# Performance work log

Hardware: AMD Instinct MI355X
Metric: run time of the kernel (lower is better)

Reference implementation:

```python
import jax, jax.numpy as jnp
import numpy as np

ALPHA = 0.2  # LeakyReLU negative slope
NEG = -9e15


def _gat_heads(x, adj_mask, W, a):
    # x: (B,N,F); W: (H,F,O); a: (H,2O); adj_mask: (B,N,N) bool
    O = W.shape[-1]
    Wh = jnp.einsum('bnf,hfo->bhno', x, W)            # (B,H,N,O)
    e1 = jnp.einsum('bhno,ho->bhn', Wh, a[:, :O])     # Wh @ a[:O]
    e2 = jnp.einsum('bhno,ho->bhn', Wh, a[:, O:])     # Wh @ a[O:]
    e = jax.nn.leaky_relu(e1[:, :, :, None] + e2[:, :, None, :], ALPHA)  # (B,H,N,N)
    e = jnp.where(adj_mask[:, None], e, NEG)
    attn = jax.nn.softmax(e, axis=-1)
    return jnp.einsum('bhnm,bhmo->bhno', attn, Wh)    # (B,H,N,O)


def _gat_block(x, adj_mask, non_pad_mask, W_heads, a_heads, W_out, a_out):
    # multi-head layer, concat=True -> elu per head, then concat on feature dim
    h = jax.nn.elu(_gat_heads(x, adj_mask, W_heads, a_heads))  # (B,H,N,O)
    B, H, N, O = h.shape
    h = jnp.transpose(h, (0, 2, 1, 3)).reshape(B, N, H * O)
    h = h * non_pad_mask
    # out layer: single head, concat=False (no inner elu)
    h = _gat_heads(h, adj_mask, W_out[None], a_out[None])[:, 0]  # (B,N,noutput)
    h = h * non_pad_mask
    return jax.nn.elu(h)


def setup_inputs() -> dict:
    key = jax.random.key(0)
    ks = jax.random.split(key, 8)
    B, N = 32, 256
    vocab, F, O, H, OUT = 200, 300, 256, 8, 512
    fea = jax.random.randint(ks[0], (B, N), 0, vocab, dtype=jnp.int32)
    adj = jax.random.randint(ks[1], (B, N, N), 0, 2, dtype=jnp.int32)
    non_pad_mask = jnp.ones((B, N, 1), dtype=jnp.float32)
    embed = jax.random.normal(ks[2], (vocab, F), dtype=jnp.float32)
    W_heads = jax.random.normal(ks[3], (H, F, O), dtype=jnp.float32) / np.sqrt(F)
    a_heads = jax.random.normal(ks[4], (H, 2 * O), dtype=jnp.float32) / np.sqrt(2 * O)
    W_out = jax.random.normal(ks[5], (H * O, OUT), dtype=jnp.float32) / np.sqrt(H * O)
    a_out = jax.random.normal(ks[6], (2 * OUT,), dtype=jnp.float32) / np.sqrt(2 * OUT)
    return {"fea": fea, "adj": adj, "non_pad_mask": non_pad_mask, "embed": embed,
            "W_heads": W_heads, "a_heads": a_heads, "W_out": W_out, "a_out": a_out}


def reference(fea, adj, non_pad_mask, embed, W_heads, a_heads, W_out, a_out):
    adj_mask = adj > 0
    x = embed[fea]  # (B,N,F)
    # GAT_num = 1; dropout is identity in eval mode
    x = _gat_block(x, adj_mask, non_pad_mask, W_heads, a_heads, W_out, a_out)
    return x  # (B, N, 512)
```

## Files before the change

kernel.cpp:

```cpp
#include <hip/hip_runtime.h>
#include <math.h>


typedef _Float16 f16;
typedef __attribute__((ext_vector_type(8))) _Float16 f16x8;
typedef __attribute__((ext_vector_type(4))) _Float16 f16x4;
typedef __attribute__((ext_vector_type(4))) float f32x4;

__device__ __forceinline__ void async16(const void* g, void* lds) {
  __builtin_amdgcn_global_load_lds(
      (const __attribute__((address_space(1))) void*)g,
      (__attribute__((address_space(3))) void*)lds, 16, 0, 0);
}

__global__ void k_prep_x(const int* __restrict__ fea, const float* __restrict__ embed,
                         f16* __restrict__ x16) {
  int row = blockIdx.x;
  int t = threadIdx.x;
  int tok = fea[row];
  float v = (t < 300) ? embed[tok * 300 + t] : 0.f;
  x16[(size_t)row * 320 + t] = (f16)v;
}

__global__ void k_prep_wc(const float* __restrict__ W, f16* __restrict__ WcT) {
  __shared__ float tile[32][33];
  int bx = blockIdx.x, by = blockIdx.y, h = blockIdx.z;
  int tid = threadIdx.x;
  int c = tid & 31, q = tid >> 5;
#pragma unroll
  for (int i = 0; i < 4; ++i) {
    int tt = q + i * 8;
    int t = bx * 32 + tt;
    float v = (t < 300) ? W[((size_t)h * 300 + t) * 256 + by * 32 + c] : 0.f;
    tile[tt][c] = v;
  }
  __syncthreads();
#pragma unroll
  for (int i = 0; i < 4; ++i) {
    int oo = q + i * 8;
    int gc = h * 256 + by * 32 + oo;
    WcT[(size_t)gc * 320 + bx * 32 + c] = (f16)tile[c][oo];
  }
}

__global__ void k_prep_wo(const float* __restrict__ W, f16* __restrict__ WoT) {
  __shared__ float tile[32][33];
  int bx = blockIdx.x, by = blockIdx.y;
  int tid = threadIdx.x;
  int c = tid & 31, q = tid >> 5;
#pragma unroll
  for (int i = 0; i < 4; ++i) {
    int kk = q + i * 8;
    tile[kk][c] = W[((size_t)bx * 32 + kk) * 512 + by * 32 + c];
  }
  __syncthreads();
#pragma unroll
  for (int i = 0; i < 4; ++i) {
    int oo = q + i * 8;
    WoT[((size_t)by * 32 + oo) * 2048 + bx * 32 + c] = (f16)tile[c][oo];
  }
}

template <int KDIM, int NCOLS>
__global__ __launch_bounds__(256, 4) void k_gemm1(const f16* __restrict__ A,
                                                  const f16* __restrict__ BT,
                                                  f16* __restrict__ outT,
                                                  const float* __restrict__ avec,
                                                  float* __restrict__ e1,
                                                  float* __restrict__ e2) {
  __shared__ f16 As[128 * 32];
  __shared__ f16 Bs[128 * 32];
  const int by = blockIdx.x, bx = blockIdx.y;
  const int tid = threadIdx.x;
  const int wave = tid >> 6, lane = tid & 63;
  const int wm = wave >> 1, wn = wave & 1;
  const int lrow = lane & 15, quad = lane >> 4;
  const int srow = lane >> 2;
  const int scol = ((lane & 3) ^ ((lane >> 3) & 3)) * 8;
  const int sq = (quad ^ ((lrow >> 1) & 3)) * 8;

  f32x4 acc[4][4] = {};
  const f16* Ag = A + (size_t)by * 128 * KDIM;
  const f16* Bg = BT + (size_t)bx * 128 * KDIM;

  for (int k0 = 0; k0 < KDIM; k0 += 32) {
    __syncthreads();
#pragma unroll
    for (int j = 0; j < 2; ++j) {
      const int r0 = wave * 32 + j * 16;
      async16(Ag + (size_t)(r0 + srow) * KDIM + k0 + scol, &As[r0 * 32]);
      async16(Bg + (size_t)(r0 + srow) * KDIM + k0 + scol, &Bs[r0 * 32]);
    }
    __syncthreads();
    f16x8 af[4], bf[4];
#pragma unroll
    for (int t = 0; t < 4; ++t) {
      af[t] = *(const f16x8*)&As[(wm * 64 + t * 16 + lrow) * 32 + sq];
      bf[t] = *(const f16x8*)&Bs[(wn * 64 + t * 16 + lrow) * 32 + sq];
    }
#pragma unroll
    for (int mt = 0; mt < 4; ++mt)
#pragma unroll
      for (int nt = 0; nt < 4; ++nt)
        acc[mt][nt] = __builtin_amdgcn_mfma_f32_16x16x32_f16(af[mt], bf[nt], acc[mt][nt], 0, 0, 0);
  }

  const int b = (by * 128) >> 8;
  const int nbase0 = (by * 128) & 255;
#pragma unroll
  for (int mt = 0; mt < 4; ++mt) {
    const int nb = nbase0 + wm * 64 + mt * 16 + quad * 4;
#pragma unroll
    for (int nt = 0; nt < 4; ++nt) {
      const int gc = bx * 128 + wn * 64 + nt * 16 + lrow;
      f16x4 v;
#pragma unroll
      for (int r = 0; r < 4; ++r) v[r] = (f16)acc[mt][nt][r];
      *(f16x4*)&outT[((size_t)b * NCOLS + gc) * 256 + nb] = v;
    }
  }

  float a1v[4], a2v[4];
#pragma unroll
  for (int nt = 0; nt < 4; ++nt) {
    const int gc = bx * 128 + wn * 64 + nt * 16 + lrow;
    int hh = gc >> 8, oo = gc & 255;
    a1v[nt] = avec[hh * 512 + oo];
    a2v[nt] = avec[hh * 512 + 256 + oo];
  }
  const int hblk = (bx * 128) >> 8;
  const int ebase = (b * 8 + hblk) * 256;
#pragma unroll
  for (int mt = 0; mt < 4; ++mt) {
    float s1[4] = {0.f, 0.f, 0.f, 0.f}, s2[4] = {0.f, 0.f, 0.f, 0.f};
#pragma unroll
    for (int nt = 0; nt < 4; ++nt)
#pragma unroll
      for (int r = 0; r < 4; ++r) {
        s1[r] += acc[mt][nt][r] * a1v[nt];
        s2[r] += acc[mt][nt][r] * a2v[nt];
      }
#pragma unroll
    for (int r = 0; r < 4; ++r)
#pragma unroll
      for (int m = 1; m < 16; m <<= 1) {
        s1[r] += __shfl_xor(s1[r], m);
        s2[r] += __shfl_xor(s2[r], m);
      }
    if (lrow == 0) {
      const int nb = nbase0 + wm * 64 + mt * 16 + quad * 4;
#pragma unroll
      for (int r = 0; r < 4; ++r) {
        atomicAdd(&e1[ebase + nb + r], s1[r]);
        atomicAdd(&e2[ebase + nb + r], s2[r]);
      }
    }
  }
}

__global__ __launch_bounds__(256, 4) void k_gemm_sk(const f16* __restrict__ A,
                                                    const f16* __restrict__ BT,
                                                    f16* __restrict__ outSK) {
  __shared__ f16 As[128 * 32];
  __shared__ f16 Bs[64 * 32];
  const int by = blockIdx.x, bx = blockIdx.y, kz = blockIdx.z;
  const int tid = threadIdx.x;
  const int wave = tid >> 6, lane = tid & 63;
  const int wm = wave >> 1, wn = wave & 1;
  const int lrow = lane & 15, quad = lane >> 4;
  const int srow = lane >> 2;
  const int scol = ((lane & 3) ^ ((lane >> 3) & 3)) * 8;
  const int sq = (quad ^ ((lrow >> 1) & 3)) * 8;

  f32x4 acc[4][2] = {};
  const f16* Ag = A + (size_t)by * 128 * 2048;
  const f16* Bg = BT + (size_t)bx * 64 * 2048;
  const int kbeg = kz * 1024;

  for (int k0 = kbeg; k0 < kbeg + 1024; k0 += 32) {
    __syncthreads();
#pragma unroll
    for (int j = 0; j < 2; ++j) {
      const int r0 = wave * 32 + j * 16;
      async16(Ag + (size_t)(r0 + srow) * 2048 + k0 + scol, &As[r0 * 32]);
    }
    {
      const int r0 = wave * 16;
      async16(Bg + (size_t)(r0 + srow) * 2048 + k0 + scol, &Bs[r0 * 32]);
    }
    __syncthreads();
    f16x8 af[4], bf[2];
#pragma unroll
    for (int t = 0; t < 4; ++t)
      af[t] = *(const f16x8*)&As[(wm * 64 + t * 16 + lrow) * 32 + sq];
#pragma unroll
    for (int t = 0; t < 2; ++t)
      bf[t] = *(const f16x8*)&Bs[(wn * 32 + t * 16 + lrow) * 32 + sq];
#pragma unroll
    for (int mt = 0; mt < 4; ++mt)
#pragma unroll
      for (int nt = 0; nt < 2; ++nt)
        acc[mt][nt] = __builtin_amdgcn_mfma_f32_16x16x32_f16(af[mt], bf[nt], acc[mt][nt], 0, 0, 0);
  }

  const int b = (by * 128) >> 8;
  const int nbase0 = (by * 128) & 255;
  f16* dst = outSK + (size_t)kz * 32 * 512 * 256;
#pragma unroll
  for (int mt = 0; mt < 4; ++mt) {
    const int nb = nbase0 + wm * 64 + mt * 16 + quad * 4;
#pragma unroll
    for (int nt = 0; nt < 2; ++nt) {
      const int gc = bx * 64 + wn * 32 + nt * 16 + lrow;
      f16x4 v;
#pragma unroll
      for (int r = 0; r < 4; ++r) v[r] = (f16)acc[mt][nt][r];
      *(f16x4*)&dst[((size_t)b * 512 + gc) * 256 + nb] = v;
    }
  }
}

__global__ void k_comb(const f16* __restrict__ sk, const float* __restrict__ ao,
                       f16* __restrict__ Wh2T, float* __restrict__ e12,
                       float* __restrict__ e22) {
  int oc = blockIdx.x;
  int b = blockIdx.y;
  int n = threadIdx.x;
  const f16* b0 = sk + ((size_t)b * 512 + oc * 64) * 256 + n;
  const f16* b1 = b0 + (size_t)32 * 512 * 256;
  f16* wbase = Wh2T + ((size_t)b * 512 + oc * 64) * 256 + n;
  float s1 = 0.f, s2 = 0.f;
#pragma unroll 8
  for (int j = 0; j < 64; ++j) {
    float v = (float)b0[(size_t)j * 256] + (float)b1[(size_t)j * 256];
    int o2 = oc * 64 + j;
    s1 += v * ao[o2];
    s2 += v * ao[512 + o2];
    wbase[(size_t)j * 256] = (f16)v;
  }
  atomicAdd(&e12[b * 256 + n], s1);
  atomicAdd(&e22[b * 256 + n], s2);
}

#define PSTRIDE 264

__global__ __launch_bounds__(256, 4) void k_attn1(
    const f16* __restrict__ WhT, const float* __restrict__ e1g, const float* __restrict__ e2g,
    const int* __restrict__ adj, const float* __restrict__ npm, f16* __restrict__ h1) {
  int h = blockIdx.x, b = blockIdx.y, nt0 = blockIdx.z;
  int bh = b * 8 + h;
  int n0 = nt0 * 64;
  __shared__ f16 P[64 * PSTRIDE];
  int tid = threadIdx.x;
  int wave = tid >> 6, lane = tid & 63;

  float4 e2v = *(const float4*)&e2g[bh * 256 + lane * 4];
  float e2m = fmaxf(fmaxf(e2v.x, e2v.y), fmaxf(e2v.z, e2v.w));
#pragma unroll
  for (int m = 1; m < 64; m <<= 1) e2m = fmaxf(e2m, __shfl_xor(e2m, m));
#pragma unroll 4
  for (int i = 0; i < 16; ++i) {
    int row = i * 4 + wave;
    int gn = b * 256 + n0 + row;
    float er = e1g[bh * 256 + n0 + row];
    float sh = er + e2m;
    sh = sh > 0.f ? sh : 0.2f * sh;
    int4 aj = *(const int4*)&adj[(size_t)gn * 256 + lane * 4];
    float p0, p1, p2, p3;
    {
      float v = er + e2v.x; v = v > 0.f ? v : 0.2f * v;
      p0 = aj.x ? __expf(v - sh) : 0.f;
      v = er + e2v.y; v = v > 0.f ? v : 0.2f * v;
      p1 = aj.y ? __expf(v - sh) : 0.f;
      v = er + e2v.z; v = v > 0.f ? v : 0.2f * v;
      p2 = aj.z ? __expf(v - sh) : 0.f;
      v = er + e2v.w; v = v > 0.f ? v : 0.2f * v;
      p3 = aj.w ? __expf(v - sh) : 0.f;
    }
    float sm = p0 + p1 + p2 + p3;
#pragma unroll
    for (int m = 1; m < 64; m <<= 1) sm += __shfl_xor(sm, m);
    float rs = 1.f / sm;
    f16x4 pw;
    pw[0] = (f16)(p0 * rs); pw[1] = (f16)(p1 * rs);
    pw[2] = (f16)(p2 * rs); pw[3] = (f16)(p3 * rs);
    *(f16x4*)&P[row * PSTRIDE + lane * 4] = pw;
  }
  __syncthreads();

  int lrow = lane & 15, quad = lane >> 4;
  f32x4 acc[4][4] = {};
  const f16* Ag = WhT + (size_t)bh * 65536;
#pragma unroll 2
  for (int k0 = 0; k0 < 256; k0 += 32) {
    f16x8 af[4], bf[4];
#pragma unroll
    for (int mt = 0; mt < 4; ++mt)
      af[mt] = *(const f16x8*)&Ag[(size_t)(wave * 64 + mt * 16 + lrow) * 256 + k0 + quad * 8];
#pragma unroll
    for (int nt = 0; nt < 4; ++nt)
      bf[nt] = *(const f16x8*)&P[(nt * 16 + lrow) * PSTRIDE + k0 + quad * 8];
#pragma unroll
    for (int mt = 0; mt < 4; ++mt)
#pragma unroll
      for (int nt = 0; nt < 4; ++nt)
        acc[mt][nt] = __builtin_amdgcn_mfma_f32_16x16x32_f16(af[mt], bf[nt], acc[mt][nt], 0, 0, 0);
  }
#pragma unroll
  for (int nt = 0; nt < 4; ++nt) {
    int nloc = nt * 16 + lrow;
    int gn = b * 256 + n0 + nloc;
    float pm = npm[gn];
#pragma unroll
    for (int mt = 0; mt < 4; ++mt) {
      int o0 = wave * 64 + mt * 16 + quad * 4;
      f16x4 st;
#pragma unroll
      for (int r = 0; r < 4; ++r) {
        float v = acc[mt][nt][r];
        v = v > 0.f ? v : (__expf(v) - 1.f);
        st[r] = (f16)(v * pm);
      }
      *(f16x4*)&h1[(size_t)gn * 2048 + h * 256 + o0] = st;
    }
  }
}

__global__ __launch_bounds__(256, 4) void k_attn2(
    const f16* __restrict__ Wh2T, const float* __restrict__ e1g, const float* __restrict__ e2g,
    const int* __restrict__ adj, const float* __restrict__ npm, float* __restrict__ out) {
  int oh = blockIdx.x, b = blockIdx.y, nt0 = blockIdx.z;
  int n0 = nt0 * 64;
  __shared__ f16 P[64 * PSTRIDE];
  int tid = threadIdx.x;
  int wave = tid >> 6, lane = tid & 63;

  float4 e2v = *(const float4*)&e2g[b * 256 + lane * 4];
  float e2m = fmaxf(fmaxf(e2v.x, e2v.y), fmaxf(e2v.z, e2v.w));
#pragma unroll
  for (int m = 1; m < 64; m <<= 1) e2m = fmaxf(e2m, __shfl_xor(e2m, m));
#pragma unroll 4
  for (int i = 0; i < 16; ++i) {
    int row = i * 4 + wave;
    int gn = b * 256 + n0 + row;
    float er = e1g[b * 256 + n0 + row];
    float sh = er + e2m;
    sh = sh > 0.f ? sh : 0.2f * sh;
    int4 aj = *(const int4*)&adj[(size_t)gn * 256 + lane * 4];
    float p0, p1, p2, p3;
    {
      float v = er + e2v.x; v = v > 0.f ? v : 0.2f * v;
      p0 = aj.x ? __expf(v - sh) : 0.f;
      v = er + e2v.y; v = v > 0.f ? v : 0.2f * v;
      p1 = aj.y ? __expf(v - sh) : 0.f;
      v = er + e2v.z; v = v > 0.f ? v : 0.2f * v;
      p2 = aj.z ? __expf(v - sh) : 0.f;
      v = er + e2v.w; v = v > 0.f ? v : 0.2f * v;
      p3 = aj.w ? __expf(v - sh) : 0.f;
    }
    float sm = p0 + p1 + p2 + p3;
#pragma unroll
    for (int m = 1; m < 64; m <<= 1) sm += __shfl_xor(sm, m);
    float rs = 1.f / sm;
    f16x4 pw;
    pw[0] = (f16)(p0 * rs); pw[1] = (f16)(p1 * rs);
    pw[2] = (f16)(p2 * rs); pw[3] = (f16)(p3 * rs);
    *(f16x4*)&P[row * PSTRIDE + lane * 4] = pw;
  }
  __syncthreads();

  int lrow = lane & 15, quad = lane >> 4;
  f32x4 acc[4][4] = {};
  const f16* Ag = Wh2T + (size_t)b * 512 * 256 + (size_t)oh * 65536;
#pragma unroll 2
  for (int k0 = 0; k0 < 256; k0 += 32) {
    f16x8 af[4], bf[4];
#pragma unroll
    for (int mt = 0; mt < 4; ++mt)
      af[mt] = *(const f16x8*)&Ag[(size_t)(wave * 64 + mt * 16 + lrow) * 256 + k0 + quad * 8];
#pragma unroll
    for (int nt = 0; nt < 4; ++nt)
      bf[nt] = *(const f16x8*)&P[(nt * 16 + lrow) * PSTRIDE + k0 + quad * 8];
#pragma unroll
    for (int mt = 0; mt < 4; ++mt)
#pragma unroll
      for (int nt = 0; nt < 4; ++nt)
        acc[mt][nt] = __builtin_amdgcn_mfma_f32_16x16x32_f16(af[mt], bf[nt], acc[mt][nt], 0, 0, 0);
  }
#pragma unroll
  for (int nt = 0; nt < 4; ++nt) {
    int nloc = nt * 16 + lrow;
    int gn = b * 256 + n0 + nloc;
    float pm = npm[gn];
#pragma unroll
    for (int mt = 0; mt < 4; ++mt) {
      int o0 = oh * 256 + wave * 64 + mt * 16 + quad * 4;
      float4 st;
      float v0 = acc[mt][nt][0] * pm;
      float v1 = acc[mt][nt][1] * pm;
      float v2 = acc[mt][nt][2] * pm;
      float v3 = acc[mt][nt][3] * pm;
      st.x = v0 > 0.f ? v0 : (__expf(v0) - 1.f);
      st.y = v1 > 0.f ? v1 : (__expf(v1) - 1.f);
      st.z = v2 > 0.f ? v2 : (__expf(v2) - 1.f);
      st.w = v3 > 0.f ? v3 : (__expf(v3) - 1.f);
      *(float4*)&out[(size_t)gn * 512 + o0] = st;
    }
  }
}

extern "C" void kernel_launch(void* const* d_in, const int* in_sizes, int n_in,
                              void* d_out, int out_size, void* d_ws, size_t ws_size,
                              hipStream_t stream) {
  (void)in_sizes; (void)n_in; (void)out_size; (void)ws_size;
  const int*   fea   = (const int*)d_in[0];
  const int*   adj   = (const int*)d_in[1];
  const float* npm   = (const float*)d_in[2];
  const float* embed = (const float*)d_in[3];
  const float* Whd   = (const float*)d_in[4];
  const float* ah    = (const float*)d_in[5];
  const float* Wo    = (const float*)d_in[6];
  const float* ao    = (const float*)d_in[7];
  float* out = (float*)d_out;

  char* ws = (char*)d_ws;
  f16* x16  = (f16*)ws;  ws += (size_t)8192 * 320 * 2;
  f16* WcT  = (f16*)ws;  ws += (size_t)2048 * 320 * 2;
  f16* WoT  = (f16*)ws;  ws += (size_t)512 * 2048 * 2;
  f16* WhT  = (f16*)ws;  ws += (size_t)32 * 8 * 256 * 256 * 2;
  f16* h1   = (f16*)ws;  ws += (size_t)8192 * 2048 * 2;
  f16* Wh2T = (f16*)ws;  ws += (size_t)32 * 512 * 256 * 2;
  f16* Wh2sk = (f16*)ws; ws += (size_t)2 * 32 * 512 * 256 * 2;
  float* e1  = (float*)ws; ws += (size_t)65536 * 4;
  float* e2  = (float*)ws; ws += (size_t)65536 * 4;
  float* e12 = (float*)ws; ws += (size_t)8192 * 4;
  float* e22 = (float*)ws; ws += (size_t)8192 * 4;

  hipMemsetAsync(e1, 0, ((size_t)65536 * 2 + 8192 * 2) * 4, stream);

  k_prep_x<<<8192, 320, 0, stream>>>(fea, embed, x16);
  k_prep_wc<<<dim3(10, 8, 8), 256, 0, stream>>>(Whd, WcT);
  k_prep_wo<<<dim3(64, 16), 256, 0, stream>>>(Wo, WoT);

  k_gemm1<320, 2048><<<dim3(64, 16), 256, 0, stream>>>(x16, WcT, WhT, ah, e1, e2);
  k_attn1<<<dim3(8, 32, 4), 256, 0, stream>>>(WhT, e1, e2, adj, npm, h1);

  k_gemm_sk<<<dim3(64, 8, 2), 256, 0, stream>>>(h1, WoT, Wh2sk);
  k_comb<<<dim3(8, 32), 256, 0, stream>>>(Wh2sk, ao, Wh2T, e12, e22);
  k_attn2<<<dim3(2, 32, 4), 256, 0, stream>>>(Wh2T, e12, e22, adj, npm, out);
}
```

Baseline: 207.5 us.

## Fuse prep kernels with memset, double GEMM K-tile to 64, widen comb grid

Merges the embedding gather, the two weight transposes and the zeroing of the e-accumulators into one launch with block-range dispatch, removing three launches and a memset. Both MFMA GEMMs now stage 64-wide K tiles with a new XOR swizzle, which halves the barrier pairs per K step at the cost of doubled LDS per block. k_comb is split into 32-column chunks so twice as many blocks run. The mixed workloads in the fused prep kernel may leave some blocks imbalanced, and the larger LDS footprint may lower occupancy.

```diff
diff --git a/kernel.cpp b/kernel.cpp
--- a/kernel.cpp
+++ b/kernel.cpp
@@ -13,51 +13,65 @@
       (__attribute__((address_space(3))) void*)lds, 16, 0, 0);
 }
 
-__global__ void k_prep_x(const int* __restrict__ fea, const float* __restrict__ embed,
-                         f16* __restrict__ x16) {
-  int row = blockIdx.x;
-  int t = threadIdx.x;
-  int tok = fea[row];
-  float v = (t < 300) ? embed[tok * 300 + t] : 0.f;
-  x16[(size_t)row * 320 + t] = (f16)v;
-}
-
-__global__ void k_prep_wc(const float* __restrict__ W, f16* __restrict__ WcT) {
-  __shared__ float tile[32][33];
-  int bx = blockIdx.x, by = blockIdx.y, h = blockIdx.z;
-  int tid = threadIdx.x;
-  int c = tid & 31, q = tid >> 5;
-#pragma unroll
-  for (int i = 0; i < 4; ++i) {
-    int tt = q + i * 8;
-    int t = bx * 32 + tt;
-    float v = (t < 300) ? W[((size_t)h * 300 + t) * 256 + by * 32 + c] : 0.f;
-    tile[tt][c] = v;
-  }
-  __syncthreads();
-#pragma unroll
-  for (int i = 0; i < 4; ++i) {
-    int oo = q + i * 8;
-    int gc = h * 256 + by * 32 + oo;
-    WcT[(size_t)gc * 320 + bx * 32 + c] = (f16)tile[c][oo];
-  }
-}
-
-__global__ void k_prep_wo(const float* __restrict__ W, f16* __restrict__ WoT) {
-  __shared__ float tile[32][33];
-  int bx = blockIdx.x, by = blockIdx.y;
-  int tid = threadIdx.x;
-  int c = tid & 31, q = tid >> 5;
-#pragma unroll
-  for (int i = 0; i < 4; ++i) {
-    int kk = q + i * 8;
-    tile[kk][c] = W[((size_t)bx * 32 + kk) * 512 + by * 32 + c];
-  }
-  __syncthreads();
-#pragma unroll
-  for (int i = 0; i < 4; ++i) {
-    int oo = q + i * 8;
-    WoT[((size_t)by * 32 + oo) * 2048 + bx * 32 + c] = (f16)tile[c][oo];
+__global__ __launch_bounds__(256) void k_prep(const int* __restrict__ fea,
+                                              const float* __restrict__ embed,
+                                              const float* __restrict__ Whd,
+                                              const float* __restrict__ Wo,
+                                              f16* __restrict__ x16,
+                                              f16* __restrict__ WcT,
+                                              f16* __restrict__ WoT,
+                                              float* __restrict__ e_all) {
+  int bid = blockIdx.x, tid = threadIdx.x;
+  if (bid < 1280) {
+    int idx = bid * 256 + tid;
+    int row = idx / 40, c = idx % 40;
+    int tok = fea[row];
+    const float* eb = embed + (size_t)tok * 300;
+    f16x8 v;
+#pragma unroll
+    for (int j = 0; j < 8; ++j) {
+      int t = c * 8 + j;
+      v[j] = (f16)((t < 300) ? eb[t] : 0.f);
+    }
+    *(f16x8*)&x16[(size_t)row * 320 + c * 8] = v;
+  } else if (bid < 1920) {
+    int r = bid - 1280;
+    int zi = r * 256 + tid;
+    if (zi < 147456) e_all[zi] = 0.f;
+    __shared__ float tile[32][33];
+    int bx = r % 10, q0 = r / 10;
+    int by = q0 % 8, h = q0 / 8;
+    int c = tid & 31, q = tid >> 5;
+#pragma unroll
+    for (int i = 0; i < 4; ++i) {
+      int tt = q + i * 8;
+      int t = bx * 32 + tt;
+      float v = (t < 300) ? Whd[((size_t)h * 300 + t) * 256 + by * 32 + c] : 0.f;
+      tile[tt][c] = v;
+    }
+    __syncthreads();
+#pragma unroll
+    for (int i = 0; i < 4; ++i) {
+      int oo = q + i * 8;
+      int gc = h * 256 + by * 32 + oo;
+      WcT[(size_t)gc * 320 + bx * 32 + c] = (f16)tile[c][oo];
+    }
+  } else {
+    int r = bid - 1920;
+    __shared__ float tile[32][33];
+    int bx = r % 64, by = r / 64;
+    int c = tid & 31, q = tid >> 5;
+#pragma unroll
+    for (int i = 0; i < 4; ++i) {
+      int kk = q + i * 8;
+      tile[kk][c] = Wo[((size_t)bx * 32 + kk) * 512 + by * 32 + c];
+    }
+    __syncthreads();
+#pragma unroll
+    for (int i = 0; i < 4; ++i) {
+      int oo = q + i * 8;
+      WoT[((size_t)by * 32 + oo) * 2048 + bx * 32 + c] = (f16)tile[c][oo];
+    }
   }
 }
 
@@ -68,41 +82,45 @@
                                                   const float* __restrict__ avec,
                                                   float* __restrict__ e1,
                                                   float* __restrict__ e2) {
-  __shared__ f16 As[128 * 32];
-  __shared__ f16 Bs[128 * 32];
+  __shared__ f16 As[128 * 64];
+  __shared__ f16 Bs[128 * 64];
   const int by = blockIdx.x, bx = blockIdx.y;
   const int tid = threadIdx.x;
   const int wave = tid >> 6, lane = tid & 63;
   const int wm = wave >> 1, wn = wave & 1;
   const int lrow = lane & 15, quad = lane >> 4;
-  const int srow = lane >> 2;
-  const int scol = ((lane & 3) ^ ((lane >> 3) & 3)) * 8;
-  const int sq = (quad ^ ((lrow >> 1) & 3)) * 8;
+  const int srow = lane >> 3;
+  const int scol = ((lane & 7) ^ (lane >> 3)) * 8;
+  const int l7 = lrow & 7;
 
   f32x4 acc[4][4] = {};
   const f16* Ag = A + (size_t)by * 128 * KDIM;
   const f16* Bg = BT + (size_t)bx * 128 * KDIM;
 
-  for (int k0 = 0; k0 < KDIM; k0 += 32) {
-    __syncthreads();
-#pragma unroll
-    for (int j = 0; j < 2; ++j) {
-      const int r0 = wave * 32 + j * 16;
-      async16(Ag + (size_t)(r0 + srow) * KDIM + k0 + scol, &As[r0 * 32]);
-      async16(Bg + (size_t)(r0 + srow) * KDIM + k0 + scol, &Bs[r0 * 32]);
-    }
-    __syncthreads();
-    f16x8 af[4], bf[4];
-#pragma unroll
-    for (int t = 0; t < 4; ++t) {
-      af[t] = *(const f16x8*)&As[(wm * 64 + t * 16 + lrow) * 32 + sq];
-      bf[t] = *(const f16x8*)&Bs[(wn * 64 + t * 16 + lrow) * 32 + sq];
-    }
-#pragma unroll
-    for (int mt = 0; mt < 4; ++mt)
-#pragma unroll
-      for (int nt = 0; nt < 4; ++nt)
-        acc[mt][nt] = __builtin_amdgcn_mfma_f32_16x16x32_f16(af[mt], bf[nt], acc[mt][nt], 0, 0, 0);
+  for (int k0 = 0; k0 < KDIM; k0 += 64) {
+    __syncthreads();
+#pragma unroll
+    for (int j = 0; j < 4; ++j) {
+      const int r0 = wave * 32 + j * 8;
+      async16(Ag + (size_t)(r0 + srow) * KDIM + k0 + scol, &As[r0 * 64]);
+      async16(Bg + (size_t)(r0 + srow) * KDIM + k0 + scol, &Bs[r0 * 64]);
+    }
+    __syncthreads();
+#pragma unroll
+    for (int s = 0; s < 2; ++s) {
+      const int sq = ((s * 4 + quad) ^ l7) * 8;
+      f16x8 af[4], bf[4];
+#pragma unroll
+      for (int t = 0; t < 4; ++t) {
+        af[t] = *(const f16x8*)&As[(wm * 64 + t * 16 + lrow) * 64 + sq];
+        bf[t] = *(const f16x8*)&Bs[(wn * 64 + t * 16 + lrow) * 64 + sq];
+      }
+#pragma unroll
+      for (int mt = 0; mt < 4; ++mt)
+#pragma unroll
+        for (int nt = 0; nt < 4; ++nt)
+          acc[mt][nt] = __builtin_amdgcn_mfma_f32_16x16x32_f16(af[mt], bf[nt], acc[mt][nt], 0, 0, 0);
+    }
   }
 
   const int b = (by * 128) >> 8;
@@ -161,46 +179,51 @@
 __global__ __launch_bounds__(256, 4) void k_gemm_sk(const f16* __restrict__ A,
                                                     const f16* __restrict__ BT,
                                                     f16* __restrict__ outSK) {
-  __shared__ f16 As[128 * 32];
-  __shared__ f16 Bs[64 * 32];
+  __shared__ f16 As[128 * 64];
+  __shared__ f16 Bs[64 * 64];
   const int by = blockIdx.x, bx = blockIdx.y, kz = blockIdx.z;
   const int tid = threadIdx.x;
   const int wave = tid >> 6, lane = tid & 63;
   const int wm = wave >> 1, wn = wave & 1;
   const int lrow = lane & 15, quad = lane >> 4;
-  const int srow = lane >> 2;
-  const int scol = ((lane & 3) ^ ((lane >> 3) & 3)) * 8;
-  const int sq = (quad ^ ((lrow >> 1) & 3)) * 8;
+  const int srow = lane >> 3;
+  const int scol = ((lane & 7) ^ (lane >> 3)) * 8;
+  const int l7 = lrow & 7;
 
   f32x4 acc[4][2] = {};
   const f16* Ag = A + (size_t)by * 128 * 2048;
   const f16* Bg = BT + (size_t)bx * 64 * 2048;
   const int kbeg = kz * 1024;
 
-  for (int k0 = kbeg; k0 < kbeg + 1024; k0 += 32) {
-    __syncthreads();
+  for (int k0 = kbeg; k0 < kbeg + 1024; k0 += 64) {
+    __syncthreads();
+#pragma unroll
+    for (int j = 0; j < 4; ++j) {
+      const int r0 = wave * 32 + j * 8;
+      async16(Ag + (size_t)(r0 + srow) * 2048 + k0 + scol, &As[r0 * 64]);
+    }
 #pragma unroll
     for (int j = 0; j < 2; ++j) {
-      const int r0 = wave * 32 + j * 16;
-      async16(Ag + (size_t)(r0 + srow) * 2048 + k0 + scol, &As[r0 * 32]);
-    }
-    {
-      const int r0 = wave * 16;
-      async16(Bg + (size_t)(r0 + srow) * 2048 + k0 + scol, &Bs[r0 * 32]);
-    }
-    __syncthreads();
-    f16x8 af[4], bf[2];
-#pragma unroll
-    for (int t = 0; t < 4; ++t)
-      af[t] = *(const f16x8*)&As[(wm * 64 + t * 16 + lrow) * 32 + sq];
-#pragma unroll
-    for (int t = 0; t < 2; ++t)
-      bf[t] = *(const f16x8*)&Bs[(wn * 32 + t * 16 + lrow) * 32 + sq];
-#pragma unroll
-    for (int mt = 0; mt < 4; ++mt)
-#pragma unroll
-      for (int nt = 0; nt < 2; ++nt)
-        acc[mt][nt] = __builtin_amdgcn_mfma_f32_16x16x32_f16(af[mt], bf[nt], acc[mt][nt], 0, 0, 0);
+      const int r0 = wave * 16 + j * 8;
+      async16(Bg + (size_t)(r0 + srow) * 2048 + k0 + scol, &Bs[r0 * 64]);
+    }
+    __syncthreads();
+#pragma unroll
+    for (int s = 0; s < 2; ++s) {
+      const int sq = ((s * 4 + quad) ^ l7) * 8;
+      f16x8 af[4], bf[2];
+#pragma unroll
+      for (int t = 0; t < 4; ++t)
+        af[t] = *(const f16x8*)&As[(wm * 64 + t * 16 + lrow) * 64 + sq];
+#pragma unroll
+      for (int t = 0; t < 2; ++t)
+        bf[t] = *(const f16x8*)&Bs[(wn * 32 + t * 16 + lrow) * 64 + sq];
+#pragma unroll
+      for (int mt = 0; mt < 4; ++mt)
+#pragma unroll
+        for (int nt = 0; nt < 2; ++nt)
+          acc[mt][nt] = __builtin_amdgcn_mfma_f32_16x16x32_f16(af[mt], bf[nt], acc[mt][nt], 0, 0, 0);
+    }
   }
 
   const int b = (by * 128) >> 8;
@@ -226,14 +249,14 @@
   int oc = blockIdx.x;
   int b = blockIdx.y;
   int n = threadIdx.x;
-  const f16* b0 = sk + ((size_t)b * 512 + oc * 64) * 256 + n;
+  const f16* b0 = sk + ((size_t)b * 512 + oc * 32) * 256 + n;
   const f16* b1 = b0 + (size_t)32 * 512 * 256;
-  f16* wbase = Wh2T + ((size_t)b * 512 + oc * 64) * 256 + n;
+  f16* wbase = Wh2T + ((size_t)b * 512 + oc * 32) * 256 + n;
   float s1 = 0.f, s2 = 0.f;
 #pragma unroll 8
-  for (int j = 0; j < 64; ++j) {
+  for (int j = 0; j < 32; ++j) {
     float v = (float)b0[(size_t)j * 256] + (float)b1[(size_t)j * 256];
-    int o2 = oc * 64 + j;
+    int o2 = oc * 32 + j;
     s1 += v * ao[o2];
     s2 += v * ao[512 + o2];
     wbase[(size_t)j * 256] = (f16)v;
@@ -436,16 +459,12 @@
   float* e12 = (float*)ws; ws += (size_t)8192 * 4;
   float* e22 = (float*)ws; ws += (size_t)8192 * 4;
 
-  hipMemsetAsync(e1, 0, ((size_t)65536 * 2 + 8192 * 2) * 4, stream);
-
-  k_prep_x<<<8192, 320, 0, stream>>>(fea, embed, x16);
-  k_prep_wc<<<dim3(10, 8, 8), 256, 0, stream>>>(Whd, WcT);
-  k_prep_wo<<<dim3(64, 16), 256, 0, stream>>>(Wo, WoT);
+  k_prep<<<2944, 256, 0, stream>>>(fea, embed, Whd, Wo, x16, WcT, WoT, e1);
 
   k_gemm1<320, 2048><<<dim3(64, 16), 256, 0, stream>>>(x16, WcT, WhT, ah, e1, e2);
   k_attn1<<<dim3(8, 32, 4), 256, 0, stream>>>(WhT, e1, e2, adj, npm, h1);
 
   k_gemm_sk<<<dim3(64, 8, 2), 256, 0, stream>>>(h1, WoT, Wh2sk);
-  k_comb<<<dim3(8, 32), 256, 0, stream>>>(Wh2sk, ao, Wh2T, e12, e22);
+  k_comb<<<dim3(16, 32), 256, 0, stream>>>(Wh2sk, ao, Wh2T, e12, e22);
   k_attn2<<<dim3(2, 32, 4), 256, 0, stream>>>(Wh2T, e12, e22, adj, npm, out);
 }
```

Result: faster. 200.1 us (-3.5%).
